# Kernel tuning notes

Hardware: AMD Instinct MI355X
Metric: run time of the kernel (lower is better)

Reference implementation:

```python
import jax, jax.numpy as jnp
import numpy as np

C_M = 256   # norm_channel (msa channel)
C_Z = 128   # pair_channel
H = 8       # num_head
C = 32      # attention_channel per head


def layer_norm(x, gamma, beta, eps=1e-5):
    mu = jnp.mean(x, axis=-1, keepdims=True)
    var = jnp.var(x, axis=-1, keepdims=True)
    return (x - mu) * jax.lax.rsqrt(var + eps) * gamma + beta


def setup_inputs() -> dict:
    key = jax.random.key(0)
    ks = jax.random.split(key, 12)
    B, S, R = 1, 128, 256
    inp = {
        "msa_act": jax.random.normal(ks[0], (B, S, R, C_M), jnp.float32),
        "pair_act": jax.random.normal(ks[1], (B, R, R, C_Z), jnp.float32),
        "msa_mask": jnp.ones((B, S, R), jnp.float32),
        # query_norm params
        "qn_g": jnp.ones((C_M,), jnp.float32),
        "qn_b": jnp.zeros((C_M,), jnp.float32),
        # feat_2d_norm params
        "pn_g": jnp.ones((C_Z,), jnp.float32),
        "pn_b": jnp.zeros((C_Z,), jnp.float32),
        # feat_2d_weights: Linear(C_Z -> H, bias=False)
        "w2d": jax.random.normal(ks[2], (C_Z, H), jnp.float32) / np.sqrt(C_Z),
        # attention projections [C_M, H, C]
        "wq": jax.random.normal(ks[3], (C_M, H, C), jnp.float32) / np.sqrt(C_M),
        "wk": jax.random.normal(ks[4], (C_M, H, C), jnp.float32) / np.sqrt(C_M),
        "wv": jax.random.normal(ks[5], (C_M, H, C), jnp.float32) / np.sqrt(C_M),
        # gating linear [C_M, H, C] + bias
        "wg": jax.random.normal(ks[6], (C_M, H, C), jnp.float32) / np.sqrt(C_M),
        "bg": jnp.ones((H, C), jnp.float32),
        # output linear [H, C, C_M] + bias
        "wo": jax.random.normal(ks[7], (H, C, C_M), jnp.float32) / np.sqrt(H * C),
        "bo": jnp.zeros((C_M,), jnp.float32),
    }
    return inp


def reference(msa_act, pair_act, msa_mask, qn_g, qn_b, pn_g, pn_b, w2d,
              wq, wk, wv, wg, bg, wo, bo):
    # Pair bias: LayerNorm -> Linear(C_Z->H) -> permute to [B, 1, H, R, R]
    z = layer_norm(pair_act, pn_g, pn_b)            # [B, R, R, C_Z]
    z = jnp.einsum('bqkc,ch->bhqk', z, w2d)          # [B, H, R, R]
    z = z[:, None]                                   # [B, 1, H, R, R]

    # Mask bias: [B, S, 1, 1, R]
    mask_bias = (1e9 * (msa_mask - 1.0))[:, :, None, None, :]

    # Row-wise MHA with query norm
    m = layer_norm(msa_act, qn_g, qn_b)              # [B, S, R, C_M]
    scale = 1.0 / np.sqrt(C)
    q = jnp.einsum('bsqc,chd->bshqd', m, wq) * scale
    k = jnp.einsum('bskc,chd->bshkd', m, wk)
    v = jnp.einsum('bskc,chd->bshkd', m, wv)

    logits = jnp.einsum('bshqd,bshkd->bshqk', q, k) + mask_bias + z
    a = jax.nn.softmax(logits, axis=-1)              # [B, S, H, R, R]
    o = jnp.einsum('bshqk,bshkd->bsqhd', a, v)       # [B, S, R, H, C]

    g = jax.nn.sigmoid(jnp.einsum('bsqc,chd->bsqhd', m, wg) + bg)
    o = o * g
    out = jnp.einsum('bsqhd,hdc->bsqc', o, wo) + bo  # [B, S, R, C_M]
    return out
```

## Files before the change

### kernel.cpp

```cpp
#include <hip/hip_runtime.h>
#include <hip/hip_bf16.h>

typedef unsigned short u16;
typedef __attribute__((ext_vector_type(8))) short bf16x8;
typedef __attribute__((ext_vector_type(4))) float f32x4;

__device__ __forceinline__ float bf2f(u16 u){
  union { unsigned int i; float f; } v; v.i = ((unsigned int)u) << 16; return v.f;
}
__device__ __forceinline__ u16 f2bf(float f){
  union { float f; unsigned int i; } v; v.f = f;
  unsigned int i = v.i;
  return (u16)((i + 0x7fffu + ((i >> 16) & 1u)) >> 16);
}
__device__ __forceinline__ unsigned int pk2(float a, float b){
  union { __hip_bfloat162 v; unsigned int u; } c;
  c.v = __float22bfloat162_rn(float2{a, b});
  return c.u;
}
__device__ __forceinline__ float ldin(const void* p, int i, int f){
  return f ? ((const float*)p)[i] : bf2f(((const u16*)p)[i]);
}

__global__ void k_sniff(const unsigned int* __restrict__ msa_w, int* __restrict__ flag)
{
  int lane = threadIdx.x & 63;
  int lo0 = 0, expok = 0;
  #pragma unroll
  for (int j = 0; j < 4; ++j) {
    unsigned int w = msa_w[lane * 4 + j];
    if ((w & 0xffffu) == 0u) lo0++;
    unsigned int e = (w >> 7) & 0xffu;
    if (e >= 110u && e <= 140u) expok++;
  }
  #pragma unroll
  for (int off = 1; off < 64; off <<= 1) {
    lo0   += __shfl_xor(lo0,   off, 64);
    expok += __shfl_xor(expok, off, 64);
  }
  if (lane == 0 && blockIdx.x == 0)
    *flag = (lo0 > 200) ? 1 : ((expok > 200) ? 0 : 1);
}

__global__ __launch_bounds__(256) void k_transpose(
    const void* __restrict__ wq, const void* __restrict__ wk,
    const void* __restrict__ wv, const void* __restrict__ wg,
    const void* __restrict__ wo, const int* __restrict__ flagp,
    u16* __restrict__ Wt, u16* __restrict__ wot)
{
  __shared__ u16 T[64 * 72];
  const int flag = *flagp;
  const int t = threadIdx.x;
  const int mat = blockIdx.x >> 4, tile = blockIdx.x & 15;
  const int R0 = (tile >> 2) * 64, C0 = (tile & 3) * 64;
  const void* src = (mat == 0) ? wq : (mat == 1) ? wk : (mat == 2) ? wv
                  : (mat == 3) ? wg : wo;
  u16* dst = (mat < 4) ? (Wt + mat * 65536) : wot;
  {
    int i = t >> 2, j0 = (t & 3) * 16;
    #pragma unroll
    for (int e = 0; e < 8; ++e) {
      float a = ldin(src, (R0 + i) * 256 + C0 + j0 + 2*e,     flag);
      float b = ldin(src, (R0 + i) * 256 + C0 + j0 + 2*e + 1, flag);
      *(unsigned int*)(T + i * 72 + j0 + 2*e) = pk2(a, b);
    }
  }
  __syncthreads();
  {
    int j = t >> 2, i0 = (t & 3) * 16;
    u16 o[16];
    #pragma unroll
    for (int e = 0; e < 16; ++e) o[e] = T[(i0 + e) * 72 + j];
    *(uint4*)(dst + (C0 + j) * 256 + R0 + i0)     = *(const uint4*)o;
    *(uint4*)(dst + (C0 + j) * 256 + R0 + i0 + 8) = *(const uint4*)(o + 8);
  }
}

__global__ __launch_bounds__(256) void k_pair_z(
    const void* __restrict__ pair, const void* __restrict__ png,
    const void* __restrict__ pnb, const void* __restrict__ w2d,
    const int* __restrict__ flagp, u16* __restrict__ z_bf)
{
  __shared__ u16 As[64 * 136];
  __shared__ u16 Bs[16 * 136];
  const int flag = *flagp;
  const int t = threadIdx.x, lane = t & 63, wave = t >> 6;
  const int g = lane >> 4, l15 = lane & 15;
  const int rowBase = blockIdx.x * 64;

  if (t < 128) {
    #pragma unroll
    for (int n = 0; n < 16; ++n)
      Bs[n * 136 + t] = (n < 8) ? f2bf(ldin(w2d, t * 8 + n, flag)) : (u16)0;
  }
  {
    int lrow = t >> 2, cb = (t & 3) * 32;
    int base = (rowBase + lrow) * 128 + cb;
    float x[32];
    if (flag) {
      const float* p = (const float*)pair + base;
      #pragma unroll
      for (int j = 0; j < 8; ++j) {
        float4 f4 = *(const float4*)(p + 4 * j);
        x[4*j] = f4.x; x[4*j+1] = f4.y; x[4*j+2] = f4.z; x[4*j+3] = f4.w;
      }
    } else {
      const u16* p = (const u16*)pair + base;
      #pragma unroll
      for (int j = 0; j < 4; ++j) {
        uint4 u = *(const uint4*)(p + 8 * j);
        const u16* h = (const u16*)&u;
        #pragma unroll
        for (int e = 0; e < 8; ++e) x[8*j+e] = bf2f(h[e]);
      }
    }
    float s = 0.f, sq = 0.f;
    #pragma unroll
    for (int j = 0; j < 32; ++j) { s += x[j]; sq += x[j] * x[j]; }
    s  += __shfl_xor(s, 1, 64);  s  += __shfl_xor(s, 2, 64);
    sq += __shfl_xor(sq, 1, 64); sq += __shfl_xor(sq, 2, 64);
    float mu = s * (1.f / 128.f);
    float var = sq * (1.f / 128.f) - mu * mu;
    float rs = rsqrtf(var + 1e-5f);
    float n_[32];
    #pragma unroll
    for (int j = 0; j < 32; ++j) {
      int c = cb + j;
      n_[j] = (x[j] - mu) * rs * ldin(png, c, flag) + ldin(pnb, c, flag);
    }
    u16* dst = As + lrow * 136 + cb;
    #pragma unroll
    for (int j = 0; j < 16; ++j)
      *(unsigned int*)(dst + 2*j) = pk2(n_[2*j], n_[2*j+1]);
  }
  __syncthreads();

  f32x4 accz = {0.f, 0.f, 0.f, 0.f};
  #pragma unroll
  for (int kb = 0; kb < 4; ++kb) {
    bf16x8 a = *(const bf16x8*)(As + (wave * 16 + l15) * 136 + kb * 32 + g * 8);
    bf16x8 b = *(const bf16x8*)(Bs + l15 * 136 + kb * 32 + g * 8);
    accz = __builtin_amdgcn_mfma_f32_16x16x32_bf16(a, b, accz, 0, 0, 0);
  }
  if (l15 < 8) {
    #pragma unroll
    for (int r = 0; r < 4; ++r)
      z_bf[l15 * 65536 + rowBase + wave * 16 + g * 4 + r] = f2bf(accz[r]);
  }
}

__global__ __launch_bounds__(256) void k_msa_ln(
    const void* __restrict__ msa, const void* __restrict__ qng,
    const void* __restrict__ qnb, const int* __restrict__ flagp,
    u16* __restrict__ m_bf)
{
  const int flag = *flagp;
  int wave = threadIdx.x >> 6, lane = threadIdx.x & 63;
  int row = blockIdx.x * 4 + wave;
  float x[4];
  if (flag) {
    float4 f4 = *((const float4*)msa + row * 64 + lane);
    x[0]=f4.x; x[1]=f4.y; x[2]=f4.z; x[3]=f4.w;
  } else {
    uint2 u = *((const uint2*)msa + row * 64 + lane);
    const u16* h = (const u16*)&u;
    #pragma unroll
    for (int j = 0; j < 4; ++j) x[j] = bf2f(h[j]);
  }
  float s = 0.f, sq = 0.f;
  #pragma unroll
  for (int j = 0; j < 4; ++j) { s += x[j]; sq += x[j] * x[j]; }
  #pragma unroll
  for (int off = 1; off < 64; off <<= 1) {
    s  += __shfl_xor(s,  off, 64);
    sq += __shfl_xor(sq, off, 64);
  }
  float mu = s * (1.f / 256.f);
  float var = sq * (1.f / 256.f) - mu * mu;
  float rs = rsqrtf(var + 1e-5f);
  float y[4];
  #pragma unroll
  for (int j = 0; j < 4; ++j) {
    int c = lane * 4 + j;
    y[j] = (x[j] - mu) * rs * ldin(qng, c, flag) + ldin(qnb, c, flag);
  }
  uint2 o2;
  o2.x = pk2(y[0], y[1]);
  o2.y = pk2(y[2], y[3]);
  *((uint2*)m_bf + row * 64 + lane) = o2;
}

__global__ __launch_bounds__(256, 2) void k_fused(
    const u16* __restrict__ m_bf, const u16* __restrict__ Wt,
    const void* __restrict__ bg, const u16* __restrict__ z_bf,
    const void* __restrict__ mask, const int* __restrict__ flagp,
    u16* __restrict__ og_ws)
{
  __shared__ u16 Ks[256 * 40];
  __shared__ u16 Vts[32 * 264];
  __shared__ float Mb[256];
  const int flag = *flagp;
  const int t = threadIdx.x, lane = t & 63, wave = t >> 6;
  const int s_ = blockIdx.x, h = blockIdx.y;
  const int g = lane >> 4, l15 = lane & 15;

  Mb[t] = 1e9f * (ldin(mask, s_ * 256 + t, flag) - 1.0f);

  const float scale = 0.17677669529663687f;
  f32x4 zero = {0.f, 0.f, 0.f, 0.f};

  bf16x8 af[8][4];
  #pragma unroll
  for (int kb = 0; kb < 8; ++kb)
    #pragma unroll
    for (int mt = 0; mt < 4; ++mt)
      af[kb][mt] = *(const bf16x8*)(
          m_bf + (s_ * 256 + wave * 64 + mt * 16 + l15) * 256 + kb * 32 + g * 8);

  unsigned int qp[4][4];
  float gg[4][2][4];

  #pragma unroll
  for (int matid = 0; matid < 4; ++matid) {
    const u16* W = Wt + matid * 65536 + (h * 32) * 256;
    f32x4 acc[4][2];
    #pragma unroll
    for (int mt = 0; mt < 4; ++mt) { acc[mt][0] = zero; acc[mt][1] = zero; }
    #pragma unroll
    for (int kb = 0; kb < 8; ++kb) {
      bf16x8 b0 = *(const bf16x8*)(W + l15 * 256        + kb * 32 + g * 8);
      bf16x8 b1 = *(const bf16x8*)(W + (16 + l15) * 256 + kb * 32 + g * 8);
      #pragma unroll
      for (int mt = 0; mt < 4; ++mt) {
        if (matid == 0 || matid == 2) {
          acc[mt][0] = __builtin_amdgcn_mfma_f32_16x16x32_bf16(b0, af[kb][mt], acc[mt][0], 0, 0, 0);
          acc[mt][1] = __builtin_amdgcn_mfma_f32_16x16x32_bf16(b1, af[kb][mt], acc[mt][1], 0, 0, 0);
        } else {
          acc[mt][0] = __builtin_amdgcn_mfma_f32_16x16x32_bf16(af[kb][mt], b0, acc[mt][0], 0, 0, 0);
          acc[mt][1] = __builtin_amdgcn_mfma_f32_16x16x32_bf16(af[kb][mt], b1, acc[mt][1], 0, 0, 0);
        }
      }
    }
    if (matid == 0) {
      #pragma unroll
      for (int mt = 0; mt < 4; ++mt) {
        qp[mt][0] = pk2(acc[mt][0][0] * scale, acc[mt][0][1] * scale);
        qp[mt][1] = pk2(acc[mt][0][2] * scale, acc[mt][0][3] * scale);
        qp[mt][2] = pk2(acc[mt][1][0] * scale, acc[mt][1][1] * scale);
        qp[mt][3] = pk2(acc[mt][1][2] * scale, acc[mt][1][3] * scale);
      }
    } else if (matid == 1) {
      #pragma unroll
      for (int mt = 0; mt < 4; ++mt)
        #pragma unroll
        for (int r = 0; r < 4; ++r) {
          int rowl = wave * 64 + mt * 16 + g * 4 + r;
          Ks[rowl * 40 + l15]      = f2bf(acc[mt][0][r]);
          Ks[rowl * 40 + 16 + l15] = f2bf(acc[mt][1][r]);
        }
    } else if (matid == 2) {
      #pragma unroll
      for (int mt = 0; mt < 4; ++mt)
        #pragma unroll
        for (int r = 0; r < 4; ++r) {
          int kcol = wave * 64 + mt * 16 + l15;
          Vts[(g * 4 + r) * 264 + kcol]      = f2bf(acc[mt][0][r]);
          Vts[(16 + g * 4 + r) * 264 + kcol] = f2bf(acc[mt][1][r]);
        }
    } else {
      #pragma unroll
      for (int mt = 0; mt < 4; ++mt)
        #pragma unroll
        for (int nt = 0; nt < 2; ++nt)
          #pragma unroll
          for (int r = 0; r < 4; ++r) {
            float gv = acc[mt][nt][r] + ldin(bg, h * 32 + nt * 16 + l15, flag);
            gg[mt][nt][r] = 1.0f / (1.0f + __expf(-gv));
          }
    }
  }
  __syncthreads();

  #pragma unroll
  for (int qt = 0; qt < 4; ++qt) {
    __builtin_amdgcn_sched_barrier(0);
    const int qbase = wave * 64 + qt * 16;
    const u16* zb = z_bf + h * 65536 + (qbase + l15) * 256;
    uint2 zu[16];
    #pragma unroll
    for (int kt = 0; kt < 16; ++kt)
      zu[kt] = *(const uint2*)(zb + kt * 16 + g * 4);

    union { bf16x8 v; unsigned int w[4]; } aq;
    aq.w[0] = qp[qt][0]; aq.w[1] = qp[qt][1];
    aq.w[2] = qp[qt][2]; aq.w[3] = qp[qt][3];

    f32x4 S[16];
    #pragma unroll
    for (int kt = 0; kt < 16; ++kt) {
      union { bf16x8 v; uint2 u2[2]; } kf;
      const u16* kr = Ks + (kt * 16 + l15) * 40;
      kf.u2[0] = *(const uint2*)(kr + g * 4);
      kf.u2[1] = *(const uint2*)(kr + 16 + g * 4);
      S[kt] = __builtin_amdgcn_mfma_f32_16x16x32_bf16(kf.v, aq.v, zero, 0, 0, 0);
    }

    float sm = 0.f;
    unsigned int pw[8][4];
    #pragma unroll
    for (int kc = 0; kc < 8; ++kc) {
      #pragma unroll
      for (int half = 0; half < 2; ++half) {
        const int kt = kc * 2 + half;
        float4 mb = *(const float4*)(Mb + kt * 16 + g * 4);
        const u16* zh = (const u16*)&zu[kt];
        float e0 = __expf(S[kt][0] + mb.x + bf2f(zh[0]));
        float e1 = __expf(S[kt][1] + mb.y + bf2f(zh[1]));
        float e2 = __expf(S[kt][2] + mb.z + bf2f(zh[2]));
        float e3 = __expf(S[kt][3] + mb.w + bf2f(zh[3]));
        sm += (e0 + e1) + (e2 + e3);
        pw[kc][half * 2]     = pk2(e0, e1);
        pw[kc][half * 2 + 1] = pk2(e2, e3);
      }
    }

    f32x4 O0a = zero, O0b = zero, O1a = zero, O1b = zero;
    #pragma unroll
    for (int kc = 0; kc < 8; ++kc) {
      union { bf16x8 v; unsigned int w[4]; } pf;
      pf.w[0] = pw[kc][0]; pf.w[1] = pw[kc][1];
      pf.w[2] = pw[kc][2]; pf.w[3] = pw[kc][3];
      union { bf16x8 v; uint2 u2[2]; } vf0, vf1;
      const u16* vr0 = Vts + l15 * 264 + kc * 32;
      const u16* vr1 = Vts + (16 + l15) * 264 + kc * 32;
      vf0.u2[0] = *(const uint2*)(vr0 + g * 4);
      vf0.u2[1] = *(const uint2*)(vr0 + 16 + g * 4);
      vf1.u2[0] = *(const uint2*)(vr1 + g * 4);
      vf1.u2[1] = *(const uint2*)(vr1 + 16 + g * 4);
      if (kc & 1) {
        O0b = __builtin_amdgcn_mfma_f32_16x16x32_bf16(pf.v, vf0.v, O0b, 0, 0, 0);
        O1b = __builtin_amdgcn_mfma_f32_16x16x32_bf16(pf.v, vf1.v, O1b, 0, 0, 0);
      } else {
        O0a = __builtin_amdgcn_mfma_f32_16x16x32_bf16(pf.v, vf0.v, O0a, 0, 0, 0);
        O1a = __builtin_amdgcn_mfma_f32_16x16x32_bf16(pf.v, vf1.v, O1a, 0, 0, 0);
      }
    }
    sm += __shfl_xor(sm, 16, 64);
    sm += __shfl_xor(sm, 32, 64);
    #pragma unroll
    for (int r = 0; r < 4; ++r) {
      float smr = __shfl(sm, g * 4 + r, 64);
      float inv = 1.0f / smr;
      int qq = qbase + g * 4 + r;
      int base = (s_ * 256 + qq) * 256 + h * 32;
      og_ws[base + l15]      = f2bf((O0a[r] + O0b[r]) * inv * gg[qt][0][r]);
      og_ws[base + 16 + l15] = f2bf((O1a[r] + O1b[r]) * inv * gg[qt][1][r]);
    }
  }
}

__global__ __launch_bounds__(256, 4) void k_outproj(
    const u16* __restrict__ og, const u16* __restrict__ wot,
    const void* __restrict__ bo, const int* __restrict__ flagp,
    void* __restrict__ outv)
{
  const int flag = *flagp;
  const int t = threadIdx.x, lane = t & 63, wave = t >> 6;
  const int wm = (wave >> 1) * 32, wn = (wave & 1) * 64;
  const int rowBase = blockIdx.x * 64;
  const int ct = blockIdx.y;
  const int g = lane >> 4, l15 = lane & 15;

  bf16x8 af[8][2];
  #pragma unroll
  for (int kb = 0; kb < 8; ++kb)
    #pragma unroll
    for (int mt = 0; mt < 2; ++mt)
      af[kb][mt] = *(const bf16x8*)(
          og + (rowBase + wm + mt * 16 + l15) * 256 + kb * 32 + g * 8);

  const u16* Wb = wot + (ct * 128 + wn) * 256;
  f32x4 acc[2][4];
  f32x4 zero = {0.f, 0.f, 0.f, 0.f};
  #pragma unroll
  for (int i = 0; i < 2; ++i)
    #pragma unroll
    for (int j = 0; j < 4; ++j) acc[i][j] = zero;
  #pragma unroll
  for (int kb = 0; kb < 8; ++kb) {
    bf16x8 bb[4];
    #pragma unroll
    for (int nt = 0; nt < 4; ++nt)
      bb[nt] = *(const bf16x8*)(Wb + (nt * 16 + l15) * 256 + kb * 32 + g * 8);
    #pragma unroll
    for (int mt = 0; mt < 2; ++mt)
      #pragma unroll
      for (int nt = 0; nt < 4; ++nt)
        acc[mt][nt] = __builtin_amdgcn_mfma_f32_16x16x32_bf16(
            af[kb][mt], bb[nt], acc[mt][nt], 0, 0, 0);
  }
  #pragma unroll
  for (int mt = 0; mt < 2; ++mt)
    #pragma unroll
    for (int nt = 0; nt < 4; ++nt)
      #pragma unroll
      for (int r = 0; r < 4; ++r) {
        int row = rowBase + wm + mt * 16 + g * 4 + r;
        int col = ct * 128 + wn + nt * 16 + l15;
        float val = acc[mt][nt][r] + ldin(bo, col, flag);
        if (flag) ((float*)outv)[row * 256 + col] = val;
        else      ((u16*)outv)[row * 256 + col]   = f2bf(val);
      }
}

extern "C" void kernel_launch(void* const* d_in, const int* in_sizes, int n_in,
                              void* d_out, int out_size, void* d_ws, size_t ws_size,
                              hipStream_t stream)
{
  const void* msa  = d_in[0];
  const void* pair = d_in[1];
  const void* mask = d_in[2];
  const void* qng  = d_in[3];
  const void* qnb  = d_in[4];
  const void* png  = d_in[5];
  const void* pnb  = d_in[6];
  const void* w2d  = d_in[7];
  const void* wq   = d_in[8];
  const void* wk   = d_in[9];
  const void* wv   = d_in[10];
  const void* wg   = d_in[11];
  const void* bg   = d_in[12];
  const void* wo   = d_in[13];
  const void* bo   = d_in[14];

  char* ws = (char*)d_ws;
  u16* z_bf  = (u16*)(ws + 0);
  u16* Wt    = (u16*)(ws + 1048576);
  u16* wot   = (u16*)(ws + 1572864);
  int* flag  = (int*)(ws + 1703936);
  u16* m_bf  = (u16*)(ws + 1704192);
  u16* og_ws = (u16*)(ws + 18481408);

  hipLaunchKernelGGL(k_sniff, dim3(1), dim3(64), 0, stream,
                     (const unsigned int*)msa, flag);
  hipLaunchKernelGGL(k_transpose, dim3(80), dim3(256), 0, stream,
                     wq, wk, wv, wg, wo, flag, Wt, wot);
  hipLaunchKernelGGL(k_msa_ln, dim3(8192), dim3(256), 0, stream,
                     msa, qng, qnb, flag, m_bf);
  hipLaunchKernelGGL(k_pair_z, dim3(1024), dim3(256), 0, stream,
                     pair, png, pnb, w2d, flag, z_bf);
  hipLaunchKernelGGL(k_fused, dim3(128, 8), dim3(256), 0, stream,
                     m_bf, Wt, bg, z_bf, mask, flag, og_ws);
  hipLaunchKernelGGL(k_outproj, dim3(512, 2), dim3(256), 0, stream,
                     og_ws, wot, bo, flag, d_out);
}
```

Before: 266.4 us.

## Merge sniff, transpose, LayerNorm and pair-bias kernels into one prep launch

Combines the dtype-sniff, weight transpose, MSA LayerNorm and pair LayerNorm+projection kernels into one block-indexed prep kernel. Each block recomputes the dtype flag locally instead of reading it from a separate launch. The goal is to cut launch overhead and inter-kernel gaps across four small launches. It also raises k_fused launch bounds from 2 to 4 waves per SIMD, which could force register spills. Every block now repeats the small sniff read, and the unified shared-memory footprint may lower occupancy for the LayerNorm blocks.

```diff
diff --git a/kernel.cpp b/kernel.cpp
--- a/kernel.cpp
+++ b/kernel.cpp
@@ -22,175 +22,173 @@
   return f ? ((const float*)p)[i] : bf2f(((const u16*)p)[i]);
 }
 
-__global__ void k_sniff(const unsigned int* __restrict__ msa_w, int* __restrict__ flag)
-{
-  int lane = threadIdx.x & 63;
-  int lo0 = 0, expok = 0;
-  #pragma unroll
-  for (int j = 0; j < 4; ++j) {
-    unsigned int w = msa_w[lane * 4 + j];
-    if ((w & 0xffffu) == 0u) lo0++;
-    unsigned int e = (w >> 7) & 0xffu;
-    if (e >= 110u && e <= 140u) expok++;
-  }
-  #pragma unroll
-  for (int off = 1; off < 64; off <<= 1) {
-    lo0   += __shfl_xor(lo0,   off, 64);
-    expok += __shfl_xor(expok, off, 64);
-  }
-  if (lane == 0 && blockIdx.x == 0)
-    *flag = (lo0 > 200) ? 1 : ((expok > 200) ? 0 : 1);
-}
-
-__global__ __launch_bounds__(256) void k_transpose(
+__global__ __launch_bounds__(256) void k_prep(
+    const void* __restrict__ msa,  const void* __restrict__ pair,
+    const void* __restrict__ qng,  const void* __restrict__ qnb,
+    const void* __restrict__ png,  const void* __restrict__ pnb,
+    const void* __restrict__ w2d,
     const void* __restrict__ wq, const void* __restrict__ wk,
     const void* __restrict__ wv, const void* __restrict__ wg,
-    const void* __restrict__ wo, const int* __restrict__ flagp,
-    u16* __restrict__ Wt, u16* __restrict__ wot)
+    const void* __restrict__ wo,
+    u16* __restrict__ Wt, u16* __restrict__ wot,
+    u16* __restrict__ m_bf, u16* __restrict__ z_bf,
+    int* __restrict__ flagp)
 {
-  __shared__ u16 T[64 * 72];
-  const int flag = *flagp;
+  __shared__ u16 shm[11008];
+  __shared__ int flag_sh;
   const int t = threadIdx.x;
-  const int mat = blockIdx.x >> 4, tile = blockIdx.x & 15;
-  const int R0 = (tile >> 2) * 64, C0 = (tile & 3) * 64;
-  const void* src = (mat == 0) ? wq : (mat == 1) ? wk : (mat == 2) ? wv
-                  : (mat == 3) ? wg : wo;
-  u16* dst = (mat < 4) ? (Wt + mat * 65536) : wot;
-  {
-    int i = t >> 2, j0 = (t & 3) * 16;
-    #pragma unroll
-    for (int e = 0; e < 8; ++e) {
-      float a = ldin(src, (R0 + i) * 256 + C0 + j0 + 2*e,     flag);
-      float b = ldin(src, (R0 + i) * 256 + C0 + j0 + 2*e + 1, flag);
-      *(unsigned int*)(T + i * 72 + j0 + 2*e) = pk2(a, b);
-    }
+  const int bid = blockIdx.x;
+
+  if (t < 64) {
+    const unsigned int* msa_w = (const unsigned int*)msa;
+    int lo0 = 0, expok = 0;
+    #pragma unroll
+    for (int j = 0; j < 4; ++j) {
+      unsigned int w = msa_w[t * 4 + j];
+      if ((w & 0xffffu) == 0u) lo0++;
+      unsigned int e = (w >> 7) & 0xffu;
+      if (e >= 110u && e <= 140u) expok++;
+    }
+    #pragma unroll
+    for (int off = 1; off < 64; off <<= 1) {
+      lo0   += __shfl_xor(lo0,   off, 64);
+      expok += __shfl_xor(expok, off, 64);
+    }
+    if (t == 0) flag_sh = (lo0 > 200) ? 1 : ((expok > 200) ? 0 : 1);
   }
   __syncthreads();
-  {
-    int j = t >> 2, i0 = (t & 3) * 16;
-    u16 o[16];
-    #pragma unroll
-    for (int e = 0; e < 16; ++e) o[e] = T[(i0 + e) * 72 + j];
-    *(uint4*)(dst + (C0 + j) * 256 + R0 + i0)     = *(const uint4*)o;
-    *(uint4*)(dst + (C0 + j) * 256 + R0 + i0 + 8) = *(const uint4*)(o + 8);
+  const int flag = flag_sh;
+  if (bid == 0 && t == 0) *flagp = flag;
+
+  if (bid < 80) {
+    u16* T = shm;
+    const int mat = bid >> 4, tile = bid & 15;
+    const int R0 = (tile >> 2) * 64, C0 = (tile & 3) * 64;
+    const void* src = (mat == 0) ? wq : (mat == 1) ? wk : (mat == 2) ? wv
+                    : (mat == 3) ? wg : wo;
+    u16* dst = (mat < 4) ? (Wt + mat * 65536) : wot;
+    {
+      int i = t >> 2, j0 = (t & 3) * 16;
+      #pragma unroll
+      for (int e = 0; e < 8; ++e) {
+        float a = ldin(src, (R0 + i) * 256 + C0 + j0 + 2*e,     flag);
+        float b = ldin(src, (R0 + i) * 256 + C0 + j0 + 2*e + 1, flag);
+        *(unsigned int*)(T + i * 72 + j0 + 2*e) = pk2(a, b);
+      }
+    }
+    __syncthreads();
+    {
+      int j = t >> 2, i0 = (t & 3) * 16;
+      u16 o[16];
+      #pragma unroll
+      for (int e = 0; e < 16; ++e) o[e] = T[(i0 + e) * 72 + j];
+      *(uint4*)(dst + (C0 + j) * 256 + R0 + i0)     = *(const uint4*)o;
+      *(uint4*)(dst + (C0 + j) * 256 + R0 + i0 + 8) = *(const uint4*)(o + 8);
+    }
+  } else if (bid < 8272) {
+    int wave = t >> 6, lane = t & 63;
+    int row = (bid - 80) * 4 + wave;
+    float x[4];
+    if (flag) {
+      float4 f4 = *((const float4*)msa + row * 64 + lane);
+      x[0]=f4.x; x[1]=f4.y; x[2]=f4.z; x[3]=f4.w;
+    } else {
+      uint2 u = *((const uint2*)msa + row * 64 + lane);
+      const u16* h = (const u16*)&u;
+      #pragma unroll
+      for (int j = 0; j < 4; ++j) x[j] = bf2f(h[j]);
+    }
+    float s = 0.f, sq = 0.f;
+    #pragma unroll
+    for (int j = 0; j < 4; ++j) { s += x[j]; sq += x[j] * x[j]; }
+    #pragma unroll
+    for (int off = 1; off < 64; off <<= 1) {
+      s  += __shfl_xor(s,  off, 64);
+      sq += __shfl_xor(sq, off, 64);
+    }
+    float mu = s * (1.f / 256.f);
+    float var = sq * (1.f / 256.f) - mu * mu;
+    float rs = rsqrtf(var + 1e-5f);
+    float y[4];
+    #pragma unroll
+    for (int j = 0; j < 4; ++j) {
+      int c = lane * 4 + j;
+      y[j] = (x[j] - mu) * rs * ldin(qng, c, flag) + ldin(qnb, c, flag);
+    }
+    uint2 o2;
+    o2.x = pk2(y[0], y[1]);
+    o2.y = pk2(y[2], y[3]);
+    *((uint2*)m_bf + row * 64 + lane) = o2;
+  } else {
+    u16* As = shm;
+    u16* Bs = shm + 64 * 136;
+    const int lane = t & 63, wave = t >> 6;
+    const int g = lane >> 4, l15 = lane & 15;
+    const int rowBase = (bid - 8272) * 64;
+
+    if (t < 128) {
+      #pragma unroll
+      for (int n = 0; n < 16; ++n)
+        Bs[n * 136 + t] = (n < 8) ? f2bf(ldin(w2d, t * 8 + n, flag)) : (u16)0;
+    }
+    {
+      int lrow = t >> 2, cb = (t & 3) * 32;
+      int base = (rowBase + lrow) * 128 + cb;
+      float x[32];
+      if (flag) {
+        const float* p = (const float*)pair + base;
+        #pragma unroll
+        for (int j = 0; j < 8; ++j) {
+          float4 f4 = *(const float4*)(p + 4 * j);
+          x[4*j] = f4.x; x[4*j+1] = f4.y; x[4*j+2] = f4.z; x[4*j+3] = f4.w;
+        }
+      } else {
+        const u16* p = (const u16*)pair + base;
+        #pragma unroll
+        for (int j = 0; j < 4; ++j) {
+          uint4 u = *(const uint4*)(p + 8 * j);
+          const u16* h = (const u16*)&u;
+          #pragma unroll
+          for (int e = 0; e < 8; ++e) x[8*j+e] = bf2f(h[e]);
+        }
+      }
+      float s = 0.f, sq = 0.f;
+      #pragma unroll
+      for (int j = 0; j < 32; ++j) { s += x[j]; sq += x[j] * x[j]; }
+      s  += __shfl_xor(s, 1, 64);  s  += __shfl_xor(s, 2, 64);
+      sq += __shfl_xor(sq, 1, 64); sq += __shfl_xor(sq, 2, 64);
+      float mu = s * (1.f / 128.f);
+      float var = sq * (1.f / 128.f) - mu * mu;
+      float rs = rsqrtf(var + 1e-5f);
+      float n_[32];
+      #pragma unroll
+      for (int j = 0; j < 32; ++j) {
+        int c = cb + j;
+        n_[j] = (x[j] - mu) * rs * ldin(png, c, flag) + ldin(pnb, c, flag);
+      }
+      u16* dst = As + lrow * 136 + cb;
+      #pragma unroll
+      for (int j = 0; j < 16; ++j)
+        *(unsigned int*)(dst + 2*j) = pk2(n_[2*j], n_[2*j+1]);
+    }
+    __syncthreads();
+
+    f32x4 accz = {0.f, 0.f, 0.f, 0.f};
+    #pragma unroll
+    for (int kb = 0; kb < 4; ++kb) {
+      bf16x8 a = *(const bf16x8*)(As + (wave * 16 + l15) * 136 + kb * 32 + g * 8);
+      bf16x8 b = *(const bf16x8*)(Bs + l15 * 136 + kb * 32 + g * 8);
+      accz = __builtin_amdgcn_mfma_f32_16x16x32_bf16(a, b, accz, 0, 0, 0);
+    }
+    if (l15 < 8) {
+      #pragma unroll
+      for (int r = 0; r < 4; ++r)
+        z_bf[l15 * 65536 + rowBase + wave * 16 + g * 4 + r] = f2bf(accz[r]);
+    }
   }
 }
 
-__global__ __launch_bounds__(256) void k_pair_z(
-    const void* __restrict__ pair, const void* __restrict__ png,
-    const void* __restrict__ pnb, const void* __restrict__ w2d,
-    const int* __restrict__ flagp, u16* __restrict__ z_bf)
-{
-  __shared__ u16 As[64 * 136];
-  __shared__ u16 Bs[16 * 136];
-  const int flag = *flagp;
-  const int t = threadIdx.x, lane = t & 63, wave = t >> 6;
-  const int g = lane >> 4, l15 = lane & 15;
-  const int rowBase = blockIdx.x * 64;
-
-  if (t < 128) {
-    #pragma unroll
-    for (int n = 0; n < 16; ++n)
-      Bs[n * 136 + t] = (n < 8) ? f2bf(ldin(w2d, t * 8 + n, flag)) : (u16)0;
-  }
-  {
-    int lrow = t >> 2, cb = (t & 3) * 32;
-    int base = (rowBase + lrow) * 128 + cb;
-    float x[32];
-    if (flag) {
-      const float* p = (const float*)pair + base;
-      #pragma unroll
-      for (int j = 0; j < 8; ++j) {
-        float4 f4 = *(const float4*)(p + 4 * j);
-        x[4*j] = f4.x; x[4*j+1] = f4.y; x[4*j+2] = f4.z; x[4*j+3] = f4.w;
-      }
-    } else {
-      const u16* p = (const u16*)pair + base;
-      #pragma unroll
-      for (int j = 0; j < 4; ++j) {
-        uint4 u = *(const uint4*)(p + 8 * j);
-        const u16* h = (const u16*)&u;
-        #pragma unroll
-        for (int e = 0; e < 8; ++e) x[8*j+e] = bf2f(h[e]);
-      }
-    }
-    float s = 0.f, sq = 0.f;
-    #pragma unroll
-    for (int j = 0; j < 32; ++j) { s += x[j]; sq += x[j] * x[j]; }
-    s  += __shfl_xor(s, 1, 64);  s  += __shfl_xor(s, 2, 64);
-    sq += __shfl_xor(sq, 1, 64); sq += __shfl_xor(sq, 2, 64);
-    float mu = s * (1.f / 128.f);
-    float var = sq * (1.f / 128.f) - mu * mu;
-    float rs = rsqrtf(var + 1e-5f);
-    float n_[32];
-    #pragma unroll
-    for (int j = 0; j < 32; ++j) {
-      int c = cb + j;
-      n_[j] = (x[j] - mu) * rs * ldin(png, c, flag) + ldin(pnb, c, flag);
-    }
-    u16* dst = As + lrow * 136 + cb;
-    #pragma unroll
-    for (int j = 0; j < 16; ++j)
-      *(unsigned int*)(dst + 2*j) = pk2(n_[2*j], n_[2*j+1]);
-  }
-  __syncthreads();
-
-  f32x4 accz = {0.f, 0.f, 0.f, 0.f};
-  #pragma unroll
-  for (int kb = 0; kb < 4; ++kb) {
-    bf16x8 a = *(const bf16x8*)(As + (wave * 16 + l15) * 136 + kb * 32 + g * 8);
-    bf16x8 b = *(const bf16x8*)(Bs + l15 * 136 + kb * 32 + g * 8);
-    accz = __builtin_amdgcn_mfma_f32_16x16x32_bf16(a, b, accz, 0, 0, 0);
-  }
-  if (l15 < 8) {
-    #pragma unroll
-    for (int r = 0; r < 4; ++r)
-      z_bf[l15 * 65536 + rowBase + wave * 16 + g * 4 + r] = f2bf(accz[r]);
-  }
-}
-
-__global__ __launch_bounds__(256) void k_msa_ln(
-    const void* __restrict__ msa, const void* __restrict__ qng,
-    const void* __restrict__ qnb, const int* __restrict__ flagp,
-    u16* __restrict__ m_bf)
-{
-  const int flag = *flagp;
-  int wave = threadIdx.x >> 6, lane = threadIdx.x & 63;
-  int row = blockIdx.x * 4 + wave;
-  float x[4];
-  if (flag) {
-    float4 f4 = *((const float4*)msa + row * 64 + lane);
-    x[0]=f4.x; x[1]=f4.y; x[2]=f4.z; x[3]=f4.w;
-  } else {
-    uint2 u = *((const uint2*)msa + row * 64 + lane);
-    const u16* h = (const u16*)&u;
-    #pragma unroll
-    for (int j = 0; j < 4; ++j) x[j] = bf2f(h[j]);
-  }
-  float s = 0.f, sq = 0.f;
-  #pragma unroll
-  for (int j = 0; j < 4; ++j) { s += x[j]; sq += x[j] * x[j]; }
-  #pragma unroll
-  for (int off = 1; off < 64; off <<= 1) {
-    s  += __shfl_xor(s,  off, 64);
-    sq += __shfl_xor(sq, off, 64);
-  }
-  float mu = s * (1.f / 256.f);
-  float var = sq * (1.f / 256.f) - mu * mu;
-  float rs = rsqrtf(var + 1e-5f);
-  float y[4];
-  #pragma unroll
-  for (int j = 0; j < 4; ++j) {
-    int c = lane * 4 + j;
-    y[j] = (x[j] - mu) * rs * ldin(qng, c, flag) + ldin(qnb, c, flag);
-  }
-  uint2 o2;
-  o2.x = pk2(y[0], y[1]);
-  o2.y = pk2(y[2], y[3]);
-  *((uint2*)m_bf + row * 64 + lane) = o2;
-}
-
-__global__ __launch_bounds__(256, 2) void k_fused(
+__global__ __launch_bounds__(256, 4) void k_fused(
     const u16* __restrict__ m_bf, const u16* __restrict__ Wt,
     const void* __restrict__ bg, const u16* __restrict__ z_bf,
     const void* __restrict__ mask, const int* __restrict__ flagp,
@@ -441,14 +439,9 @@
   u16* m_bf  = (u16*)(ws + 1704192);
   u16* og_ws = (u16*)(ws + 18481408);
 
-  hipLaunchKernelGGL(k_sniff, dim3(1), dim3(64), 0, stream,
-                     (const unsigned int*)msa, flag);
-  hipLaunchKernelGGL(k_transpose, dim3(80), dim3(256), 0, stream,
-                     wq, wk, wv, wg, wo, flag, Wt, wot);
-  hipLaunchKernelGGL(k_msa_ln, dim3(8192), dim3(256), 0, stream,
-                     msa, qng, qnb, flag, m_bf);
-  hipLaunchKernelGGL(k_pair_z, dim3(1024), dim3(256), 0, stream,
-                     pair, png, pnb, w2d, flag, z_bf);
+  hipLaunchKernelGGL(k_prep, dim3(9296), dim3(256), 0, stream,
+                     msa, pair, qng, qnb, png, pnb, w2d,
+                     wq, wk, wv, wg, wo, Wt, wot, m_bf, z_bf, flag);
   hipLaunchKernelGGL(k_fused, dim3(128, 8), dim3(256), 0, stream,
                      m_bf, Wt, bg, z_bf, mask, flag, og_ws);
   hipLaunchKernelGGL(k_outproj, dim3(512, 2), dim3(256), 0, stream,
```

New measurement: 373.7 us. +40.2%, slower.
